# Performance work log

Hardware: AMD Instinct MI355X
Metric: run time of the kernel (lower is better)

## Reference

```python
import jax, jax.numpy as jnp
import numpy as np

BETA_MEM = 0.9
BETA_INH = 0.6
THRESHOLD = 1.0  # snn.Leaky default


def setup_inputs() -> dict:
    key = jax.random.key(0)
    k1, = jax.random.split(key, 1)
    T, B = 1024, 16384
    spike_seq = (jax.random.uniform(k1, (T, B, 2)) < 0.05).astype(jnp.float32)
    w_exc = jnp.array([[0.7, 1.0]], dtype=jnp.float32)  # fc_exc.weight, [1, 2]
    w_inh = jnp.array(-1.0, dtype=jnp.float32)          # scalar inhibitory weight
    return {"spike_seq": spike_seq, "w_exc": w_exc, "w_inh": w_inh}


@jax.custom_vjp
def spike_fn(x):
    # Heaviside spike with ATan surrogate gradient (snntorch default, alpha=2)
    return (x > 0).astype(x.dtype)

def _spike_fwd(x):
    return spike_fn(x), x

def _spike_bwd(x, g):
    return (g / (1.0 + (jnp.pi * x) ** 2),)

spike_fn.defvjp(_spike_fwd, _spike_bwd)


def reference(spike_seq, w_exc, w_inh):
    T, B, _ = spike_seq.shape
    mem0 = jnp.zeros((B, 1), dtype=spike_seq.dtype)
    inh0 = jnp.zeros((B, 1), dtype=spike_seq.dtype)

    def step(carry, x_t):
        mem, inh = carry
        cur_exc = x_t @ w_exc.T                      # [B, 1]
        fm1 = x_t[:, 0:1]                            # [B, 1]
        inh = BETA_INH * inh + fm1
        cur = cur_exc + w_inh * inh
        # snn.Leaky: reset (subtract) computed from previous mem, detached
        reset = jax.lax.stop_gradient((mem - THRESHOLD > 0).astype(mem.dtype))
        mem = BETA_MEM * mem + cur - reset * THRESHOLD
        spk = spike_fn(mem - THRESHOLD)
        return (mem, inh), (spk, mem)

    _, (spk_rec, mem_rec) = jax.lax.scan(step, (mem0, inh0), spike_seq)
    return spk_rec, mem_rec  # each [T, B, 1]
```

## Files before the change

### kernel.cpp

```cpp
#include <hip/hip_runtime.h>

#define T_LEN 1024
#define B_N   16384
#define UNROLL 16

__global__ __launch_bounds__(64, 1) void FMFMNeuronInhib_34033320854098_kernel(
    const float* __restrict__ x,
    const float* __restrict__ w_exc,
    const float* __restrict__ w_inh,
    float* __restrict__ out) {
#pragma clang fp contract(off)
  const int b = blockIdx.x * 64 + threadIdx.x;
  const float w0 = w_exc[0];
  const float w1 = w_exc[1];
  const float wi = w_inh[0];

  float* __restrict__ spk_out = out;
  float* __restrict__ mem_out = out + (size_t)T_LEN * B_N;
  const float2* __restrict__ xp = (const float2*)x;

  float mem = 0.0f;
  float inh = 0.0f;

  float2 cur_buf[UNROLL];
  float2 nxt_buf[UNROLL];

#pragma unroll
  for (int u = 0; u < UNROLL; ++u) cur_buf[u] = xp[u * B_N + b];

  for (int t0 = 0; t0 < T_LEN; t0 += UNROLL) {
    const int t1 = t0 + UNROLL;
    if (t1 < T_LEN) {
#pragma unroll
      for (int u = 0; u < UNROLL; ++u) nxt_buf[u] = xp[(t1 + u) * B_N + b];
    }
#pragma unroll
    for (int u = 0; u < UNROLL; ++u) {
      const int t = t0 + u;
      const float x0 = cur_buf[u].x;
      const float x1 = cur_buf[u].y;
      const float cur_exc = x0 * w0 + x1 * w1;
      inh = 0.6f * inh + x0;
      const float cur = cur_exc + wi * inh;
      const float reset = (mem - 1.0f > 0.0f) ? 1.0f : 0.0f;
      mem = 0.9f * mem + cur - reset * 1.0f;
      const float spk = (mem - 1.0f > 0.0f) ? 1.0f : 0.0f;
      spk_out[t * B_N + b] = spk;
      mem_out[t * B_N + b] = mem;
    }
#pragma unroll
    for (int u = 0; u < UNROLL; ++u) cur_buf[u] = nxt_buf[u];
  }
}

extern "C" void kernel_launch(void* const* d_in, const int* in_sizes, int n_in,
                              void* d_out, int out_size, void* d_ws, size_t ws_size,
                              hipStream_t stream) {
  const float* x     = (const float*)d_in[0];
  const float* w_exc = (const float*)d_in[1];
  const float* w_inh = (const float*)d_in[2];
  float* out = (float*)d_out;

  dim3 grid(B_N / 64);
  dim3 block(64);
  hipLaunchKernelGGL(FMFMNeuronInhib_34033320854098_kernel, grid, block, 0, stream,
                     x, w_exc, w_inh, out);
}
```

Baseline: 257.6 us.

## Split scan into carry pass and chunk-parallel emit pass

Replaces the single serial pass with two kernels. The first walks the full time sequence per batch element and records mem/inh state at each of 32 chunk boundaries in the workspace. The second launches one block per chunk and batch tile, recomputes each chunk from its saved state, and writes the outputs with nontemporal stores. The aim is to expose far more parallelism for the output-heavy phase, at the cost of reading the input twice and running an extra serial pass.

```diff
diff --git a/kernel.cpp b/kernel.cpp
--- a/kernel.cpp
+++ b/kernel.cpp
@@ -1,55 +1,87 @@
 #include <hip/hip_runtime.h>
 
-#define T_LEN 1024
-#define B_N   16384
-#define UNROLL 16
+#define T_LEN  1024
+#define B_N    16384
+#define CHUNKS 32
+#define CLEN   (T_LEN / CHUNKS)
+#define D_PF   32
 
-__global__ __launch_bounds__(64, 1) void FMFMNeuronInhib_34033320854098_kernel(
-    const float* __restrict__ x,
-    const float* __restrict__ w_exc,
-    const float* __restrict__ w_inh,
+__device__ __forceinline__ void neuron_step(float x0, float x1,
+                                            float w0, float w1, float wi,
+                                            float& mem, float& inh, float& spk) {
+#pragma clang fp contract(off)
+  const float cur_exc = x0 * w0 + x1 * w1;
+  inh = 0.6f * inh + x0;
+  const float cur = cur_exc + wi * inh;
+  const float reset = (mem - 1.0f > 0.0f) ? 1.0f : 0.0f;
+  mem = 0.9f * mem + cur - reset * 1.0f;
+  spk = (mem - 1.0f > 0.0f) ? 1.0f : 0.0f;
+}
+
+__global__ __launch_bounds__(64, 1) void FMFM_phase1_carry(
+    const float* __restrict__ x, const float* __restrict__ w_exc,
+    const float* __restrict__ w_inh, float* __restrict__ carry) {
+#pragma clang fp contract(off)
+  const int b = blockIdx.x * 64 + threadIdx.x;
+  const float w0 = w_exc[0], w1 = w_exc[1], wi = w_inh[0];
+  const float2* __restrict__ xp = (const float2*)x;
+
+  float mem = 0.0f, inh = 0.0f;
+  float spk;
+
+  float2 buf[D_PF];
+#pragma unroll
+  for (int u = 0; u < D_PF; ++u) buf[u] = xp[u * B_N + b];
+
+  for (int t0 = 0; t0 < T_LEN - D_PF; t0 += D_PF) {
+    const int c = t0 / CLEN;
+    carry[c * B_N + b] = mem;
+    carry[CHUNKS * B_N + c * B_N + b] = inh;
+#pragma unroll
+    for (int u = 0; u < D_PF; ++u) {
+      const float2 v = buf[u];
+      buf[u] = xp[(t0 + u + D_PF) * B_N + b];
+      neuron_step(v.x, v.y, w0, w1, wi, mem, inh, spk);
+    }
+  }
+  {
+    const int t0 = T_LEN - D_PF;
+    const int c = t0 / CLEN;
+    carry[c * B_N + b] = mem;
+    carry[CHUNKS * B_N + c * B_N + b] = inh;
+#pragma unroll
+    for (int u = 0; u < D_PF; ++u)
+      neuron_step(buf[u].x, buf[u].y, w0, w1, wi, mem, inh, spk);
+  }
+}
+
+__global__ __launch_bounds__(256) void FMFM_phase2_emit(
+    const float* __restrict__ x, const float* __restrict__ w_exc,
+    const float* __restrict__ w_inh, const float* __restrict__ carry,
     float* __restrict__ out) {
 #pragma clang fp contract(off)
-  const int b = blockIdx.x * 64 + threadIdx.x;
-  const float w0 = w_exc[0];
-  const float w1 = w_exc[1];
-  const float wi = w_inh[0];
+  const int c = blockIdx.x >> 6;
+  const int b = ((blockIdx.x & 63) << 8) + threadIdx.x;
+  const float w0 = w_exc[0], w1 = w_exc[1], wi = w_inh[0];
+  const float2* __restrict__ xp = (const float2*)x;
+
+  float mem = carry[c * B_N + b];
+  float inh = carry[CHUNKS * B_N + c * B_N + b];
+  const int tbase = c * CLEN;
+
+  float2 buf[CLEN];
+#pragma unroll
+  for (int u = 0; u < CLEN; ++u) buf[u] = xp[(tbase + u) * B_N + b];
 
   float* __restrict__ spk_out = out;
   float* __restrict__ mem_out = out + (size_t)T_LEN * B_N;
-  const float2* __restrict__ xp = (const float2*)x;
-
-  float mem = 0.0f;
-  float inh = 0.0f;
-
-  float2 cur_buf[UNROLL];
-  float2 nxt_buf[UNROLL];
-
+  float spk;
 #pragma unroll
-  for (int u = 0; u < UNROLL; ++u) cur_buf[u] = xp[u * B_N + b];
-
-  for (int t0 = 0; t0 < T_LEN; t0 += UNROLL) {
-    const int t1 = t0 + UNROLL;
-    if (t1 < T_LEN) {
-#pragma unroll
-      for (int u = 0; u < UNROLL; ++u) nxt_buf[u] = xp[(t1 + u) * B_N + b];
-    }
-#pragma unroll
-    for (int u = 0; u < UNROLL; ++u) {
-      const int t = t0 + u;
-      const float x0 = cur_buf[u].x;
-      const float x1 = cur_buf[u].y;
-      const float cur_exc = x0 * w0 + x1 * w1;
-      inh = 0.6f * inh + x0;
-      const float cur = cur_exc + wi * inh;
-      const float reset = (mem - 1.0f > 0.0f) ? 1.0f : 0.0f;
-      mem = 0.9f * mem + cur - reset * 1.0f;
-      const float spk = (mem - 1.0f > 0.0f) ? 1.0f : 0.0f;
-      spk_out[t * B_N + b] = spk;
-      mem_out[t * B_N + b] = mem;
-    }
-#pragma unroll
-    for (int u = 0; u < UNROLL; ++u) cur_buf[u] = nxt_buf[u];
+  for (int u = 0; u < CLEN; ++u) {
+    const int t = tbase + u;
+    neuron_step(buf[u].x, buf[u].y, w0, w1, wi, mem, inh, spk);
+    __builtin_nontemporal_store(spk, &spk_out[t * B_N + b]);
+    __builtin_nontemporal_store(mem, &mem_out[t * B_N + b]);
   }
 }
 
@@ -59,10 +91,11 @@
   const float* x     = (const float*)d_in[0];
   const float* w_exc = (const float*)d_in[1];
   const float* w_inh = (const float*)d_in[2];
-  float* out = (float*)d_out;
+  float* out   = (float*)d_out;
+  float* carry = (float*)d_ws;
 
-  dim3 grid(B_N / 64);
-  dim3 block(64);
-  hipLaunchKernelGGL(FMFMNeuronInhib_34033320854098_kernel, grid, block, 0, stream,
-                     x, w_exc, w_inh, out);
+  hipLaunchKernelGGL(FMFM_phase1_carry, dim3(B_N / 64), dim3(64), 0, stream,
+                     x, w_exc, w_inh, carry);
+  hipLaunchKernelGGL(FMFM_phase2_emit, dim3(CHUNKS * (B_N / 256)), dim3(256), 0,
+                     stream, x, w_exc, w_inh, carry, out);
 }
```

Result: slower. 279.4 us (+8.5%).
